# Kernel optimization log

Measured on AMD Instinct MI355X. Metric: run time of the kernel, lower is better.

The kernel has to match this reference:

```python
import jax, jax.numpy as jnp
import numpy as np

B, L, PD, DIM, H, DH, DEPTH, MLP, NIMG, NCLS, TH = 2, 2048, 768, 512, 8, 64, 2, 2048, 4, 1000, 32


def _ln(x, g):
    # bias-free LayerNorm (beta buffer is zeros), eps matches torch F.layer_norm
    mu = jnp.mean(x, axis=-1, keepdims=True)
    var = jnp.var(x, axis=-1, keepdims=True)
    return (x - mu) / jnp.sqrt(var + 1e-5) * g


def _rms(x, g):
    # F.normalize(dim=-1) * sqrt(dim_head) * gamma; x: [b,h,n,dh], g: [h,1,dh]
    n = jnp.linalg.norm(x, axis=-1, keepdims=True)
    return x / jnp.maximum(n, 1e-12) * (DH ** 0.5) * g


def _attn(x, context, mask, ln_g, qg, kg, Wq, Wkv, Wo):
    b, n = x.shape[0], x.shape[1]
    xn = _ln(x, ln_g)
    kv = xn if context is None else context  # context is NOT pre-normed (matches source)
    m = kv.shape[1]
    q = (xn @ Wq).reshape(b, n, H, DH).transpose(0, 2, 1, 3)   # [b,h,n,dh]
    k, v = jnp.split(kv @ Wkv, 2, axis=-1)
    k = k.reshape(b, m, H, DH).transpose(0, 2, 1, 3)
    v = v.reshape(b, m, H, DH).transpose(0, 2, 1, 3)
    q = _rms(q, qg)
    k = _rms(k, kg)
    dots = jnp.einsum('bhid,bhjd->bhij', q, k)  # no 1/sqrt(d): QK-RMSNorm carries the scale
    neg = -jnp.finfo(dots.dtype).max
    dots = jnp.where(mask, dots, neg)
    a = jax.nn.softmax(dots, axis=-1)
    out = jnp.einsum('bhij,bhjd->bhid', a, v)
    out = out.transpose(0, 2, 1, 3).reshape(b, n, H * DH)
    return out @ Wo


def _forward(patches, ln_pe1_g, W_pe, b_pe, ln_pe2_g, pos_h_emb, pos_w_emb,
             attn_ln_g, q_g, k_g, Wq, Wkv, Wo, ff_ln_g, W1, b1, W2, b2,
             final_ln_g, pool_q, pool_ln_g, pool_q_g, pool_k_g,
             pool_Wq, pool_Wkv, pool_Wo, head_ln_g, W_head,
             pos_h, pos_w, image_ids):
    # patch embedding: LN -> Linear -> LN, then factorized 2D pos embed
    x = _ln(patches, ln_pe1_g) @ W_pe + b_pe
    x = _ln(x, ln_pe2_g)
    x = x + pos_h_emb[pos_h] + pos_w_emb[pos_w]
    # block-diagonal attention mask: tokens attend only within their image
    mask = (image_ids[:, None, :, None] == image_ids[:, None, None, :])  # [B,1,L,L]
    for i in range(DEPTH):
        x = _attn(x, None, mask, attn_ln_g[i], q_g[i], k_g[i], Wq[i], Wkv[i], Wo[i]) + x
        h = _ln(x, ff_ln_g[i]) @ W1[i] + b1[i]
        h = jax.nn.gelu(h, approximate=False)
        x = h @ W2[i] + b2[i] + x
    x = _ln(x, final_ln_g)
    # attention pooling: one learned query per packed image
    queries = jnp.broadcast_to(pool_q, (B, NIMG, DIM))
    pmask = (jnp.arange(NIMG)[None, None, :, None] == image_ids[:, None, None, :])  # [B,1,NIMG,L]
    pooled = _attn(queries, x, pmask, pool_ln_g, pool_q_g, pool_k_g, pool_Wq, pool_Wkv, pool_Wo) + queries
    return _ln(pooled, head_ln_g) @ W_head  # [B, NIMG, NCLS]


def setup_inputs() -> dict:
    key = jax.random.key(0)
    ks = jax.random.split(key, 16)
    s = 0.02
    inp = {}
    inp['patches'] = jax.random.normal(ks[0], (B, L, PD), jnp.float32)
    inp['pos_h'] = jax.random.randint(ks[1], (B, L), 0, TH)
    inp['pos_w'] = jax.random.randint(ks[2], (B, L), 0, TH)
    inp['image_ids'] = jnp.sort(jax.random.randint(ks[3], (B, L), 0, NIMG), axis=-1)
    inp['ln_pe1_g'] = jnp.ones((PD,), jnp.float32)
    inp['W_pe'] = jax.random.normal(ks[4], (PD, DIM), jnp.float32) * s
    inp['b_pe'] = jnp.zeros((DIM,), jnp.float32)
    inp['ln_pe2_g'] = jnp.ones((DIM,), jnp.float32)
    inp['pos_h_emb'] = jax.random.normal(ks[5], (TH, DIM), jnp.float32)
    inp['pos_w_emb'] = jax.random.normal(ks[6], (TH, DIM), jnp.float32)
    inp['attn_ln_g'] = jnp.ones((DEPTH, DIM), jnp.float32)
    inp['q_g'] = jnp.ones((DEPTH, H, 1, DH), jnp.float32)
    inp['k_g'] = jnp.ones((DEPTH, H, 1, DH), jnp.float32)
    inp['Wq'] = jax.random.normal(ks[7], (DEPTH, DIM, H * DH), jnp.float32) * s
    inp['Wkv'] = jax.random.normal(ks[8], (DEPTH, DIM, 2 * H * DH), jnp.float32) * s
    inp['Wo'] = jax.random.normal(ks[9], (DEPTH, H * DH, DIM), jnp.float32) * s
    inp['ff_ln_g'] = jnp.ones((DEPTH, DIM), jnp.float32)
    inp['W1'] = jax.random.normal(ks[10], (DEPTH, DIM, MLP), jnp.float32) * s
    inp['b1'] = jnp.zeros((DEPTH, MLP), jnp.float32)
    inp['W2'] = jax.random.normal(ks[11], (DEPTH, MLP, DIM), jnp.float32) * s
    inp['b2'] = jnp.zeros((DEPTH, DIM), jnp.float32)
    inp['final_ln_g'] = jnp.ones((DIM,), jnp.float32)
    inp['pool_q'] = jax.random.normal(ks[12], (DIM,), jnp.float32)
    inp['pool_ln_g'] = jnp.ones((DIM,), jnp.float32)
    inp['pool_q_g'] = jnp.ones((H, 1, DH), jnp.float32)
    inp['pool_k_g'] = jnp.ones((H, 1, DH), jnp.float32)
    inp['pool_Wq'] = jax.random.normal(ks[13], (DIM, H * DH), jnp.float32) * s
    inp['pool_Wkv'] = jax.random.normal(ks[14], (DIM, 2 * H * DH), jnp.float32) * s
    inp['pool_Wo'] = jax.random.normal(ks[15], (H * DH, DIM), jnp.float32) * s
    inp['head_ln_g'] = jnp.ones((DIM,), jnp.float32)
    inp['W_head'] = jax.random.normal(jax.random.fold_in(key, 99), (DIM, NCLS), jnp.float32) * s
    return inp


def reference(patches, pos_h, pos_w, image_ids, ln_pe1_g, W_pe, b_pe, ln_pe2_g,
              pos_h_emb, pos_w_emb, attn_ln_g, q_g, k_g, Wq, Wkv, Wo, ff_ln_g,
              W1, b1, W2, b2, final_ln_g, pool_q, pool_ln_g, pool_q_g, pool_k_g,
              pool_Wq, pool_Wkv, pool_Wo, head_ln_g, W_head):
    return _forward(patches, ln_pe1_g, W_pe, b_pe, ln_pe2_g, pos_h_emb, pos_w_emb,
                    attn_ln_g, q_g, k_g, Wq, Wkv, Wo, ff_ln_g, W1, b1, W2, b2,
                    final_ln_g, pool_q, pool_ln_g, pool_q_g, pool_k_g,
                    pool_Wq, pool_Wkv, pool_Wo, head_ln_g, W_head,
                    pos_h, pos_w, image_ids)
```

## Files before the change

kernel.cpp:

```cpp
#include <hip/hip_runtime.h>
#include <hip/hip_bf16.h>
#include <cfloat>
#include <math.h>

#define BB 2
#define LL 2048
#define PD 768
#define DIM 512
#define HH 8
#define DH 64
#define DEPTH 2
#define MLP 2048
#define NIMG 4
#define NCLS 1000
#define ROWS (BB*LL)
#define NEGBIG (-1e30f)

typedef __hip_bfloat16 bf16;
typedef __bf16 v8bf __attribute__((ext_vector_type(8)));
typedef float f32x4 __attribute__((ext_vector_type(4)));

__device__ __forceinline__ float ldin(const void* p, size_t i, int bf) {
    return bf ? __bfloat162float(((const bf16*)p)[i]) : ((const float*)p)[i];
}
__device__ __forceinline__ float lda(const float* p, size_t i) { return p[i]; }
__device__ __forceinline__ float lda(const bf16* p, size_t i) { return __bfloat162float(p[i]); }
__device__ __forceinline__ void st(float* p, size_t i, float v) { p[i] = v; }
__device__ __forceinline__ void st(bf16* p, size_t i, float v) { p[i] = __float2bfloat16(v); }
__device__ __forceinline__ unsigned short f2bf(float x) {
    return __builtin_bit_cast(unsigned short, __float2bfloat16(x));
}
__device__ __forceinline__ float us2f(unsigned short u) {
    return __bfloat162float(__builtin_bit_cast(bf16, u));
}

__device__ __forceinline__ void stage16(const void* gsrc, void* ldst)
{
    __builtin_amdgcn_global_load_lds(
        (const __attribute__((address_space(1))) unsigned int*)(unsigned long long)gsrc,
        (__attribute__((address_space(3))) unsigned int*)(unsigned int)(unsigned long long)ldst,
        16, 0, 0);
}

__global__ void detect_dtype_kernel(const void* ones, int* flag)
{
    if (threadIdx.x == 0 && blockIdx.x == 0)
        *flag = (((const unsigned*)ones)[0] == 0x3F803F80u) ? 1 : 0;
}

__global__ void wconv_kernel(const void* __restrict__ W, int K, int N,
                             bf16* __restrict__ out, const int* dtf)
{
    __shared__ float t[32][33];
    const int bf = *dtf;
    const size_t zoff = (size_t)blockIdx.z * K * N;
    const int kb = blockIdx.y * 32, nb = blockIdx.x * 32;
    const int tx = threadIdx.x, ty = threadIdx.y;
    #pragma unroll
    for (int u = 0; u < 4; ++u)
        t[ty + 8 * u][tx] = ldin(W, zoff + (size_t)(kb + ty + 8 * u) * N + nb + tx, bf);
    __syncthreads();
    #pragma unroll
    for (int u = 0; u < 4; ++u)
        out[zoff + (size_t)(nb + ty + 8 * u) * K + kb + tx] = __float2bfloat16(t[tx][ty + 8 * u]);
}

template<int RAWIN, typename TOUT>
__global__ void ln_kernel(const void* __restrict__ in, const void* __restrict__ g, size_t goff,
                          TOUT* __restrict__ out, int D, const int* dtf)
{
    __shared__ float red[16];
    const int bf = *dtf;
    const int row = blockIdx.x, tid = threadIdx.x;
    const size_t base = (size_t)row * D;
    float s = 0.f, ss = 0.f;
    for (int d = tid; d < D; d += blockDim.x) {
        float v = RAWIN ? ldin(in, base + d, bf) : ((const float*)in)[base + d];
        s += v; ss += v * v;
    }
    for (int o = 32; o; o >>= 1) { s += __shfl_xor(s, o); ss += __shfl_xor(ss, o); }
    const int wid = tid >> 6, lane = tid & 63, nw = blockDim.x >> 6;
    if (lane == 0) { red[wid] = s; red[8 + wid] = ss; }
    __syncthreads();
    if (tid == 0) {
        float a = 0.f, b = 0.f;
        for (int w = 0; w < nw; ++w) { a += red[w]; b += red[8 + w]; }
        red[0] = a; red[8] = b;
    }
    __syncthreads();
    const float mean = red[0] / D;
    const float var  = red[8] / D - mean * mean;
    const float rstd = rsqrtf(var + 1e-5f);
    for (int d = tid; d < D; d += blockDim.x) {
        float v = RAWIN ? ldin(in, base + d, bf) : ((const float*)in)[base + d];
        st(out, base + d, (v - mean) * rstd * ldin(g, goff + d, bf));
    }
}

__global__ void ln_pos_kernel(float* __restrict__ x, const void* __restrict__ g,
                              const void* __restrict__ phe, const void* __restrict__ pwe,
                              const int* __restrict__ ph, const int* __restrict__ pw,
                              const int* dtf)
{
    __shared__ float red[16];
    const int bf = *dtf;
    const int row = blockIdx.x, tid = threadIdx.x;
    const size_t base = (size_t)row * DIM;
    float s = 0.f, ss = 0.f;
    for (int d = tid; d < DIM; d += 256) { float v = x[base + d]; s += v; ss += v * v; }
    for (int o = 32; o; o >>= 1) { s += __shfl_xor(s, o); ss += __shfl_xor(ss, o); }
    const int wid = tid >> 6, lane = tid & 63;
    if (lane == 0) { red[wid] = s; red[8 + wid] = ss; }
    __syncthreads();
    if (tid == 0) {
        float a = 0.f, b = 0.f;
        for (int w = 0; w < 4; ++w) { a += red[w]; b += red[8 + w]; }
        red[0] = a; red[8] = b;
    }
    __syncthreads();
    const float mean = red[0] / DIM;
    const float var  = red[8] / DIM - mean * mean;
    const float rstd = rsqrtf(var + 1e-5f);
    const size_t hoff = (size_t)ph[row] * DIM, woff = (size_t)pw[row] * DIM;
    for (int d = tid; d < DIM; d += 256) {
        float v = (x[base + d] - mean) * rstd * ldin(g, d, bf)
                + ldin(phe, hoff + d, bf) + ldin(pwe, woff + d, bf);
        x[base + d] = v;
    }
}

#define GM 128
#define GN 64
#define GK 64

template<typename TO, int EPI>
__global__ void mgemm_kernel(const bf16* __restrict__ A, const bf16* __restrict__ Wt,
                             const void* __restrict__ bias, size_t boff,
                             const float* __restrict__ resid, TO* __restrict__ out,
                             int M, int N, int K, int kc, int gelu, const int* dtf)
{
    __shared__ __align__(16) unsigned short As[GM][GK];
    __shared__ __align__(16) unsigned short Bs[GN][GK];
    const int tid = threadIdx.x;
    const int w = tid >> 6, l = tid & 63, g = l >> 4, c = l & 15;
    const int wm = (w >> 1) * 64, wn = (w & 1) * 32;
    const int m0 = blockIdx.y * GM, n0 = blockIdx.x * GN;
    const int kbeg = blockIdx.z * kc, kend = kbeg + kc;
    const int lrow = l >> 3, lcol = (l & 7) * 8;

    f32x4 acc[4][2] = {};

    for (int k0 = kbeg; k0 < kend; k0 += GK) {
        __syncthreads();
        #pragma unroll
        for (int u = 0; u < 4; ++u) {
            const int rr = 32 * w + 8 * u;
            stage16(A + (size_t)(m0 + rr + lrow) * K + k0 + lcol, &As[rr][0]);
        }
        #pragma unroll
        for (int u = 0; u < 2; ++u) {
            const int rr = 16 * w + 8 * u;
            stage16(Wt + (size_t)(n0 + rr + lrow) * K + k0 + lcol, &Bs[rr][0]);
        }
        __syncthreads();
        #pragma unroll
        for (int kk = 0; kk < GK; kk += 32) {
            v8bf av[4], bv[2];
            #pragma unroll
            for (int i = 0; i < 4; ++i) av[i] = *(const v8bf*)&As[wm + i * 16 + c][kk + 8 * g];
            #pragma unroll
            for (int j = 0; j < 2; ++j) bv[j] = *(const v8bf*)&Bs[wn + j * 16 + c][kk + 8 * g];
            #pragma unroll
            for (int i = 0; i < 4; ++i)
                #pragma unroll
                for (int j = 0; j < 2; ++j)
                    acc[i][j] = __builtin_amdgcn_mfma_f32_16x16x32_bf16(av[i], bv[j], acc[i][j], 0, 0, 0);
        }
    }

    if (EPI == 0) {
        float* po = (float*)out + (size_t)blockIdx.z * M * N;
        #pragma unroll
        for (int i = 0; i < 4; ++i) {
            const int rb = m0 + wm + i * 16 + 4 * g;
            #pragma unroll
            for (int j = 0; j < 2; ++j) {
                const int col = n0 + wn + j * 16 + c;
                #pragma unroll
                for (int r = 0; r < 4; ++r)
                    po[(size_t)(rb + r) * N + col] = acc[i][j][r];
            }
        }
    } else {
        const int bf = *dtf;
        #pragma unroll
        for (int i = 0; i < 4; ++i) {
            const int rb = m0 + wm + i * 16 + 4 * g;
            #pragma unroll
            for (int j = 0; j < 2; ++j) {
                const int col = n0 + wn + j * 16 + c;
                const float bvl = bias ? ldin(bias, boff + col, bf) : 0.f;
                #pragma unroll
                for (int r = 0; r < 4; ++r) {
                    float v = acc[i][j][r] + bvl;
                    if (gelu) v = 0.5f * v * (1.f + erff(v * 0.70710678118654752f));
                    if (resid) v += resid[(size_t)(rb + r) * N + col];
                    st(out, (size_t)(rb + r) * N + col, v);
                }
            }
        }
    }
}

template<typename TO>
__global__ void mcomb_kernel(const float* __restrict__ part, int S, const void* __restrict__ bias,
                             size_t boff, const float* __restrict__ resid, TO* __restrict__ out,
                             size_t MN, int N, int gelu, const int* dtf)
{
    const size_t idx = (size_t)blockIdx.x * 256 + threadIdx.x;
    if (idx >= MN) return;
    float v = 0.f;
    for (int s = 0; s < S; ++s) v += part[(size_t)s * MN + idx];
    const int bf = *dtf;
    if (bias) v += ldin(bias, boff + (int)(idx % N), bf);
    if (gelu) v = 0.5f * v * (1.f + erff(v * 0.70710678118654752f));
    if (resid) v += resid[idx];
    st(out, idx, v);
}

__global__ void comb_ln_kernel(const float* __restrict__ part, int S,
                               const void* __restrict__ bias, size_t boff,
                               float* __restrict__ x, const void* __restrict__ g, size_t goff,
                               bf16* __restrict__ xb, const int* dtf)
{
    __shared__ float red[16];
    const int bf = *dtf;
    const int row = blockIdx.x, tid = threadIdx.x;
    const size_t base = (size_t)row * DIM;
    float v[2];
    float s = 0.f, ss = 0.f;
    #pragma unroll
    for (int u = 0; u < 2; ++u) {
        const int d = tid + 256 * u;
        float a = 0.f;
        for (int sc = 0; sc < S; ++sc) a += part[(size_t)sc * ROWS * DIM + base + d];
        if (bias) a += ldin(bias, boff + d, bf);
        a += x[base + d];
        x[base + d] = a;
        v[u] = a; s += a; ss += a * a;
    }
    for (int o = 32; o; o >>= 1) { s += __shfl_xor(s, o); ss += __shfl_xor(ss, o); }
    const int wid = tid >> 6, lane = tid & 63;
    if (lane == 0) { red[wid] = s; red[8 + wid] = ss; }
    __syncthreads();
    if (tid == 0) {
        float a = 0.f, b = 0.f;
        for (int w2 = 0; w2 < 4; ++w2) { a += red[w2]; b += red[8 + w2]; }
        red[0] = a; red[8] = b;
    }
    __syncthreads();
    const float mean = red[0] / DIM;
    const float var  = red[8] / DIM - mean * mean;
    const float rstd = rsqrtf(var + 1e-5f);
    #pragma unroll
    for (int u = 0; u < 2; ++u) {
        const int d = tid + 256 * u;
        xb[base + d] = __float2bfloat16((v[u] - mean) * rstd * ldin(g, goff + d, bf));
    }
}

#define TS 16
template<typename TA, typename TO>
__global__ void gemm_kernel(const TA* __restrict__ A, const void* __restrict__ W, size_t woff,
                            const void* __restrict__ bias, size_t boff,
                            const float* __restrict__ resid, TO* __restrict__ out,
                            int M, int N, int K, int gelu, const int* dtf)
{
    __shared__ float As[TS][TS + 1];
    __shared__ float Bs[TS][TS + 1];
    const int bf = *dtf;
    const int tx = threadIdx.x, ty = threadIdx.y;
    const int col = blockIdx.x * TS + tx;
    const int row = blockIdx.y * TS + ty;
    float acc = 0.f;
    for (int k0 = 0; k0 < K; k0 += TS) {
        const int ka = k0 + tx;
        As[ty][tx] = (row < M && ka < K) ? lda(A, (size_t)row * K + ka) : 0.f;
        const int kb = k0 + ty;
        Bs[ty][tx] = (col < N && kb < K) ? ldin(W, woff + (size_t)kb * N + col, bf) : 0.f;
        __syncthreads();
        #pragma unroll
        for (int kk = 0; kk < TS; ++kk) acc = fmaf(As[ty][kk], Bs[kk][tx], acc);
        __syncthreads();
    }
    if (row < M && col < N) {
        if (bias) acc += ldin(bias, boff + col, bf);
        if (gelu) acc = 0.5f * acc * (1.f + erff(acc * 0.70710678118654752f));
        if (resid) acc += resid[(size_t)row * N + col];
        st(out, (size_t)row * N + col, acc);
    }
}

__global__ void rms_kernel(float* __restrict__ buf, const void* __restrict__ g, size_t goff,
                           int stride, int colbase, const int* dtf)
{
    const int bf = *dtf;
    const int r = blockIdx.x, h = blockIdx.y, lane = threadIdx.x;
    float* p = buf + (size_t)r * stride + colbase + h * DH;
    const float v = p[lane];
    float ss = v * v;
    for (int o = 32; o; o >>= 1) ss += __shfl_xor(ss, o);
    const float norm = sqrtf(ss);
    const float sc = 8.0f / fmaxf(norm, 1e-12f);
    p[lane] = v * sc * ldin(g, goff + h * DH + lane, bf);
}

__global__ void rms2_kernel(bf16* __restrict__ buf, int stride,
                            const void* __restrict__ g0, size_t g0off,
                            int base1, const void* __restrict__ g1, size_t g1off,
                            int nslot, const int* dtf)
{
    const int bf = *dtf;
    const int tid = threadIdx.x;
    const int s = tid >> 4, li = tid & 15;
    if (s >= nslot) return;
    const int h = s & 7;
    const int colbase = (s < 8) ? 0 : base1;
    const void* g = (s < 8) ? g0 : g1;
    const size_t go = ((s < 8) ? g0off : g1off) + h * DH + li * 4;
    bf16* p = buf + (size_t)blockIdx.x * stride + colbase + h * DH + li * 4;
    ushort4 v = *(const ushort4*)p;
    const float f0 = us2f(v.x), f1 = us2f(v.y), f2 = us2f(v.z), f3 = us2f(v.w);
    float ss = f0 * f0 + f1 * f1 + f2 * f2 + f3 * f3;
    ss += __shfl_xor(ss, 8); ss += __shfl_xor(ss, 4);
    ss += __shfl_xor(ss, 2); ss += __shfl_xor(ss, 1);
    const float sc = 8.0f / fmaxf(sqrtf(ss), 1e-12f);
    ushort4 o;
    o.x = f2bf(f0 * sc * ldin(g, go + 0, bf));
    o.y = f2bf(f1 * sc * ldin(g, go + 1, bf));
    o.z = f2bf(f2 * sc * ldin(g, go + 2, bf));
    o.w = f2bf(f3 * sc * ldin(g, go + 3, bf));
    *(ushort4*)p = o;
}

#define QT 64
#define KT 64
#define LP 72

__global__ void flash_attn_kernel(const bf16* __restrict__ q, int qstr,
                                  const bf16* __restrict__ kpt, const bf16* __restrict__ vpt,
                                  int kvstr, const int* __restrict__ ids,
                                  bf16* __restrict__ out)
{
    __shared__ __align__(16) unsigned short Qs[QT][LP];
    __shared__ __align__(16) unsigned short Ks[KT][LP];
    __shared__ __align__(16) unsigned short Vt[DH][LP];
    __shared__ __align__(16) unsigned short Ps[QT][LP];
    __shared__ __align__(16) int ids_s[KT];
    __shared__ __align__(16) int qids_s[QT];
    __shared__ int range_s[2];

    const int tid = threadIdx.x;
    const int h = blockIdx.y, b = blockIdx.z;
    const int qb = blockIdx.x * QT;
    const int w = tid >> 6, l = tid & 63, g = l >> 4, c = l & 15;

    {
        const int r = tid >> 2, c0 = (tid & 3) << 4;
        const bf16* qp = q + (size_t)(b * LL + qb + r) * qstr + h * DH + c0;
        *(int4*)&Qs[r][c0]     = *(const int4*)qp;
        *(int4*)&Qs[r][c0 + 8] = *(const int4*)(qp + 8);
        if (tid < QT) qids_s[tid] = ids[b * LL + qb + tid];
    }
    if (tid == 0) {
        const int* bp = ids + b * LL;
        const int qlo = bp[qb], qhi = bp[qb + QT - 1];
        int lo = 0, hi = LL;
        while (lo < hi) { int mid = (lo + hi) >> 1; if (bp[mid] < qlo) lo = mid + 1; else hi = mid; }
        range_s[0] = lo;
        int lo2 = 0, hi2 = LL;
        while (lo2 < hi2) { int mid = (lo2 + hi2) >> 1; if (bp[mid] <= qhi) lo2 = mid + 1; else hi2 = mid; }
        range_s[1] = lo2;
    }
    __syncthreads();

    const int myid = qids_s[16 * w + c];
    const v8bf qf0 = *(const v8bf*)&Qs[16 * w + c][8 * g];
    const v8bf qf1 = *(const v8bf*)&Qs[16 * w + c][8 * g + 32];
    const int kb_start = (range_s[0] / KT) * KT;
    const int kb_end = range_s[1];

    f32x4 o[4];
    #pragma unroll
    for (int dt = 0; dt < 4; ++dt) o[dt] = (f32x4){0.f, 0.f, 0.f, 0.f};
    float mr = NEGBIG, lr = 0.f;

    for (int kb = kb_start; kb < kb_end; kb += KT) {
        __syncthreads();
        {
            const int r = tid >> 2, c0 = (tid & 3) << 4;
            const bf16* kp = kpt + (size_t)(b * LL + kb + r) * kvstr + h * DH + c0;
            *(int4*)&Ks[r][c0]     = *(const int4*)kp;
            *(int4*)&Ks[r][c0 + 8] = *(const int4*)(kp + 8);
        }
        {
            const int kp2 = (tid & 31) * 2, db = (tid >> 5) * 8;
            const bf16* v0p = vpt + (size_t)(b * LL + kb + kp2) * kvstr + h * DH + db;
            const bf16* v1p = v0p + kvstr;
            const ushort4 a0 = *(const ushort4*)v0p;
            const ushort4 a1 = *(const ushort4*)(v0p + 4);
            const ushort4 b0 = *(const ushort4*)v1p;
            const ushort4 b1 = *(const ushort4*)(v1p + 4);
            const unsigned short* ap0 = (const unsigned short*)&a0;
            const unsigned short* ap1 = (const unsigned short*)&a1;
            const unsigned short* bp0 = (const unsigned short*)&b0;
            const unsigned short* bp1 = (const unsigned short*)&b1;
            #pragma unroll
            for (int j = 0; j < 4; ++j) {
                *(unsigned int*)&Vt[db + j][kp2]     = (unsigned)ap0[j] | ((unsigned)bp0[j] << 16);
                *(unsigned int*)&Vt[db + 4 + j][kp2] = (unsigned)ap1[j] | ((unsigned)bp1[j] << 16);
            }
        }
        if (tid < KT) ids_s[tid] = ids[b * LL + kb + tid];
        __syncthreads();

        f32x4 stt[4];
        #pragma unroll
        for (int t = 0; t < 4; ++t) {
            stt[t] = (f32x4){0.f, 0.f, 0.f, 0.f};
            v8bf kf0 = *(const v8bf*)&Ks[16 * t + c][8 * g];
            v8bf kf1 = *(const v8bf*)&Ks[16 * t + c][8 * g + 32];
            stt[t] = __builtin_amdgcn_mfma_f32_16x16x32_bf16(kf0, qf0, stt[t], 0, 0, 0);
            stt[t] = __builtin_amdgcn_mfma_f32_16x16x32_bf16(kf1, qf1, stt[t], 0, 0, 0);
        }

        float sv[16]; int mk[16];
        float tmax = NEGBIG;
        #pragma unroll
        for (int t = 0; t < 4; ++t) {
            int4 iv = *(const int4*)&ids_s[16 * t + 4 * g];
            const int* ivp = (const int*)&iv;
            #pragma unroll
            for (int r = 0; r < 4; ++r) {
                float s = stt[t][r];
                int m = (ivp[r] == myid);
                sv[4 * t + r] = s; mk[4 * t + r] = m;
                if (m) tmax = fmaxf(tmax, s);
            }
        }
        tmax = fmaxf(tmax, __shfl_xor(tmax, 16));
        tmax = fmaxf(tmax, __shfl_xor(tmax, 32));
        const float mnew = fmaxf(mr, tmax);
        const float al = __expf(mr - mnew);
        float tsum = 0.f;
        #pragma unroll
        for (int t = 0; t < 4; ++t) {
            ushort4 pk;
            unsigned short* pp = (unsigned short*)&pk;
            #pragma unroll
            for (int r = 0; r < 4; ++r) {
                float p = mk[4 * t + r] ? __expf(sv[4 * t + r] - mnew) : 0.f;
                tsum += p;
                pp[r] = f2bf(p);
            }
            *(ushort4*)&Ps[16 * w + c][16 * t + 4 * g] = pk;
        }
        tsum += __shfl_xor(tsum, 16);
        tsum += __shfl_xor(tsum, 32);
        lr = lr * al + tsum;
        mr = mnew;

        const float a0 = __shfl(al, 4 * g + 0);
        const float a1 = __shfl(al, 4 * g + 1);
        const float a2 = __shfl(al, 4 * g + 2);
        const float a3 = __shfl(al, 4 * g + 3);
        #pragma unroll
        for (int dt = 0; dt < 4; ++dt) {
            o[dt][0] *= a0; o[dt][1] *= a1; o[dt][2] *= a2; o[dt][3] *= a3;
        }

        const v8bf pf0 = *(const v8bf*)&Ps[16 * w + c][8 * g];
        const v8bf pf1 = *(const v8bf*)&Ps[16 * w + c][8 * g + 32];
        #pragma unroll
        for (int dt = 0; dt < 4; ++dt) {
            v8bf vf0 = *(const v8bf*)&Vt[16 * dt + c][8 * g];
            v8bf vf1 = *(const v8bf*)&Vt[16 * dt + c][8 * g + 32];
            o[dt] = __builtin_amdgcn_mfma_f32_16x16x32_bf16(pf0, vf0, o[dt], 0, 0, 0);
            o[dt] = __builtin_amdgcn_mfma_f32_16x16x32_bf16(pf1, vf1, o[dt], 0, 0, 0);
        }
    }

    const float li0 = 1.f / __shfl(lr, 4 * g + 0);
    const float li1 = 1.f / __shfl(lr, 4 * g + 1);
    const float li2 = 1.f / __shfl(lr, 4 * g + 2);
    const float li3 = 1.f / __shfl(lr, 4 * g + 3);
    #pragma unroll
    for (int dt = 0; dt < 4; ++dt) {
        bf16* op = out + (size_t)(b * LL + qb + 16 * w) * DIM + h * DH + 16 * dt + c;
        op[(size_t)(4 * g + 0) * DIM] = __float2bfloat16(o[dt][0] * li0);
        op[(size_t)(4 * g + 1) * DIM] = __float2bfloat16(o[dt][1] * li1);
        op[(size_t)(4 * g + 2) * DIM] = __float2bfloat16(o[dt][2] * li2);
        op[(size_t)(4 * g + 3) * DIM] = __float2bfloat16(o[dt][3] * li3);
    }
}

#define PCH 16
#define PCK (LL / PCH)

__global__ void pool_attn_part_kernel(const float* __restrict__ q, const bf16* __restrict__ kv,
                                      int kvs, const int* __restrict__ ids,
                                      float* __restrict__ ppm, float* __restrict__ ppl,
                                      float* __restrict__ ppo)
{
    const int iq = blockIdx.x & (NIMG - 1), ch = blockIdx.x >> 2;
    const int h = blockIdx.y, b = blockIdx.z;
    const int tid = threadIdx.x;
    const int qrow = b * NIMG + iq;
    const int j0 = ch * PCK;
    __shared__ float qs[DH];
    __shared__ float s[PCK];

    qs[tid] = q[(size_t)qrow * DIM + h * DH + tid];
    __syncthreads();
    #pragma unroll
    for (int u = 0; u < 2; ++u) {
        const int j = j0 + tid + 64 * u;
        const bf16* kp = kv + (size_t)(b * LL + j) * kvs + h * DH;
        float d = 0.f;
        #pragma unroll
        for (int t = 0; t < DH; t += 8) {
            int4 kvv = *(const int4*)&kp[t];
            const unsigned short* uu = (const unsigned short*)&kvv;
            #pragma unroll
            for (int z = 0; z < 8; ++z) d = fmaf(qs[t + z], us2f(uu[z]), d);
        }
        s[tid + 64 * u] = (ids[b * LL + j] == iq) ? d : NEGBIG;
    }
    __syncthreads();
    float m = fmaxf(s[tid], s[tid + 64]);
    for (int o = 32; o; o >>= 1) m = fmaxf(m, __shfl_xor(m, o));
    const float p0 = __expf(s[tid] - m), p1 = __expf(s[tid + 64] - m);
    float ls = p0 + p1;
    for (int o = 32; o; o >>= 1) ls += __shfl_xor(ls, o);
    s[tid] = p0; s[tid + 64] = p1;
    __syncthreads();
    float acc = 0.f;
    for (int jj = 0; jj < PCK; ++jj)
        acc += s[jj] * __bfloat162float(kv[(size_t)(b * LL + j0 + jj) * kvs + DIM + h * DH + tid]);
    const int p = ((b * HH + h) * NIMG + iq) * PCH + ch;
    if (tid == 0) { ppm[p] = m; ppl[p] = ls; }
    ppo[(size_t)p * DH + tid] = acc;
}

__global__ void pool_attn_comb_kernel(const float* __restrict__ ppm, const float* __restrict__ ppl,
                                      const float* __restrict__ ppo, float* __restrict__ out)
{
    const int iq = blockIdx.x, h = blockIdx.y, b = blockIdx.z;
    const int d = threadIdx.x;
    const int pb = ((b * HH + h) * NIMG + iq) * PCH;
    float mstar = NEGBIG;
    #pragma unroll
    for (int ch = 0; ch < PCH; ++ch) mstar = fmaxf(mstar, ppm[pb + ch]);
    float lsum = 0.f, osum = 0.f;
    #pragma unroll
    for (int ch = 0; ch < PCH; ++ch) {
        const float w = __expf(ppm[pb + ch] - mstar);
        lsum += ppl[pb + ch] * w;
        osum += ppo[(size_t)(pb + ch) * DH + d] * w;
    }
    out[(size_t)(b * NIMG + iq) * DIM + h * DH + d] = osum / lsum;
}

__global__ void fill_q_kernel(float* __restrict__ queries, const void* __restrict__ pool_q,
                              const int* dtf)
{
    const int bf = *dtf;
    const int idx = blockIdx.x * blockDim.x + threadIdx.x;
    if (idx < BB * NIMG * DIM) queries[idx] = ldin(pool_q, idx % DIM, bf);
}

__global__ void write_out_kernel(const float* __restrict__ in, void* __restrict__ out, int n,
                                 const int* dtf)
{
    const int bf = *dtf;
    const int idx = blockIdx.x * blockDim.x + threadIdx.x;
    if (idx < n) {
        if (bf) ((bf16*)out)[idx] = __float2bfloat16(in[idx]);
        else    ((float*)out)[idx] = in[idx];
    }
}

extern "C" void kernel_launch(void* const* d_in, const int* in_sizes, int n_in,
                              void* d_out, int out_size, void* d_ws, size_t ws_size,
                              hipStream_t stream)
{
    const void* patches   = d_in[0];
    const int*  pos_h     = (const int*) d_in[1];
    const int*  pos_w     = (const int*) d_in[2];
    const int*  image_ids = (const int*) d_in[3];
    const void* ln_pe1_g  = d_in[4];
    const void* W_pe      = d_in[5];
    const void* b_pe      = d_in[6];
    const void* ln_pe2_g  = d_in[7];
    const void* pos_h_emb = d_in[8];
    const void* pos_w_emb = d_in[9];
    const void* attn_ln_g = d_in[10];
    const void* q_g       = d_in[11];
    const void* k_g       = d_in[12];
    const void* Wq        = d_in[13];
    const void* Wkv       = d_in[14];
    const void* Wo        = d_in[15];
    const void* ff_ln_g   = d_in[16];
    const void* W1        = d_in[17];
    const void* b1        = d_in[18];
    const void* W2        = d_in[19];
    const void* b2        = d_in[20];
    const void* final_ln_g= d_in[21];
    const void* pool_q    = d_in[22];
    const void* pool_ln_g = d_in[23];
    const void* pool_q_g  = d_in[24];
    const void* pool_k_g  = d_in[25];
    const void* pool_Wq   = d_in[26];
    const void* pool_Wkv  = d_in[27];
    const void* pool_Wo   = d_in[28];
    const void* head_ln_g = d_in[29];
    const void* W_head    = d_in[30];

    char* p = (char*)d_ws;
    int* flag = (int*)p;                         p += 256;
    float* x   = (float*)p;                      p += (size_t)ROWS * DIM * 4;
    bf16* xb   = (bf16*)p;                       p += (size_t)ROWS * PD * 2;
    bf16* qkvb = (bf16*)p;  bf16* hb = qkvb;     p += (size_t)ROWS * MLP * 2;
    bf16* wpeT  = (bf16*)p;                      p += (size_t)DIM * PD * 2;
    bf16* wqT   = (bf16*)p;                      p += (size_t)DEPTH * DIM * DIM * 2;
    bf16* wkvT  = (bf16*)p;                      p += (size_t)DEPTH * 2 * DIM * DIM * 2;
    bf16* woT   = (bf16*)p;                      p += (size_t)DEPTH * DIM * DIM * 2;
    bf16* w1T   = (bf16*)p;                      p += (size_t)DEPTH * MLP * DIM * 2;
    bf16* w2T   = (bf16*)p;                      p += (size_t)DEPTH * DIM * MLP * 2;
    bf16* pkvT  = (bf16*)p;                      p += (size_t)2 * DIM * DIM * 2;
    float* queries = (float*)p;                  p += 4096 * 4;
    float* qp      = (float*)p;                  p += 4096 * 4;
    float* pattn   = (float*)p;                  p += 4096 * 4;
    float* pooled  = (float*)p;                  p += 4096 * 4;
    bf16*  pln     = (bf16*)p;                   p += 4096 * 2;
    float* hout    = (float*)p;                  p += 8192 * 4;
    float* ppm     = (float*)p;                  p += 1024 * 4;
    float* ppl     = (float*)p;                  p += 1024 * 4;
    float* ppo     = (float*)p;                  p += (size_t)1024 * DH * 4;
    float* part    = (float*)p;                  p += (size_t)4 * ROWS * DIM * 4;

    const dim3 blk256(256);
    const dim3 blkG(TS, TS);
    const dim3 blkT(32, 8);

    detect_dtype_kernel<<<1, 1, 0, stream>>>(ln_pe1_g, flag);

    wconv_kernel<<<dim3(DIM / 32, PD / 32, 1), blkT, 0, stream>>>(W_pe, PD, DIM, wpeT, flag);
    wconv_kernel<<<dim3(DIM / 32, DIM / 32, DEPTH), blkT, 0, stream>>>(Wq, DIM, DIM, wqT, flag);
    wconv_kernel<<<dim3(2 * DIM / 32, DIM / 32, DEPTH), blkT, 0, stream>>>(Wkv, DIM, 2 * DIM, wkvT, flag);
    wconv_kernel<<<dim3(DIM / 32, DIM / 32, DEPTH), blkT, 0, stream>>>(Wo, DIM, DIM, woT, flag);
    wconv_kernel<<<dim3(MLP / 32, DIM / 32, DEPTH), blkT, 0, stream>>>(W1, DIM, MLP, w1T, flag);
    wconv_kernel<<<dim3(DIM / 32, MLP / 32, DEPTH), blkT, 0, stream>>>(W2, MLP, DIM, w2T, flag);
    wconv_kernel<<<dim3(2 * DIM / 32, DIM / 32, 1), blkT, 0, stream>>>(pool_Wkv, DIM, 2 * DIM, pkvT, flag);

    ln_kernel<1, bf16><<<ROWS, blk256, 0, stream>>>(patches, ln_pe1_g, 0, xb, PD, flag);
    mgemm_kernel<float, 0><<<dim3(DIM / GN, ROWS / GM, 2), blk256, 0, stream>>>(
        xb, wpeT, nullptr, 0, nullptr, part, ROWS, DIM, PD, PD / 2, 0, flag);
    mcomb_kernel<float><<<(ROWS * DIM + 255) / 256, blk256, 0, stream>>>(
        part, 2, b_pe, 0, nullptr, x, (size_t)ROWS * DIM, DIM, 0, flag);
    ln_pos_kernel<<<ROWS, blk256, 0, stream>>>(x, ln_pe2_g, pos_h_emb, pos_w_emb, pos_h, pos_w, flag);
    ln_kernel<0, bf16><<<ROWS, blk256, 0, stream>>>(x, attn_ln_g, 0, xb, DIM, flag);

    for (int i = 0; i < DEPTH; ++i) {
        mgemm_kernel<bf16, 1><<<dim3(DIM / GN, ROWS / GM, 1), blk256, 0, stream>>>(
            xb, wqT + (size_t)i * DIM * DIM, nullptr, 0, nullptr, qkvb,
            ROWS, DIM, DIM, DIM, 0, flag);
        mgemm_kernel<bf16, 1><<<dim3(2 * DIM / GN, ROWS / GM, 1), blk256, 0, stream>>>(
            xb, wkvT + (size_t)i * 2 * DIM * DIM, nullptr, 0, nullptr, qkvb + (size_t)ROWS * DIM,
            ROWS, 2 * DIM, DIM, DIM, 0, flag);
        rms2_kernel<<<ROWS, blk256, 0, stream>>>(
            qkvb, DIM, q_g, (size_t)i * HH * DH, 0, nullptr, 0, 8, flag);
        rms2_kernel<<<ROWS, blk256, 0, stream>>>(
            qkvb + (size_t)ROWS * DIM, 2 * DIM, k_g, (size_t)i * HH * DH, 0, nullptr, 0, 8, flag);
        flash_attn_kernel<<<dim3(LL / QT, HH, BB), blk256, 0, stream>>>(
            qkvb, DIM, qkvb + (size_t)ROWS * DIM, qkvb + (size_t)ROWS * DIM + DIM, 2 * DIM,
            image_ids, xb);
        mgemm_kernel<float, 0><<<dim3(DIM / GN, ROWS / GM, 2), blk256, 0, stream>>>(
            xb, woT + (size_t)i * DIM * DIM, nullptr, 0, nullptr, part,
            ROWS, DIM, DIM, DIM / 2, 0, flag);
        comb_ln_kernel<<<ROWS, blk256, 0, stream>>>(
            part, 2, nullptr, 0, x, ff_ln_g, (size_t)i * DIM, xb, flag);
        mgemm_kernel<bf16, 1><<<dim3(MLP / GN, ROWS / GM, 1), blk256, 0, stream>>>(
            xb, w1T + (size_t)i * MLP * DIM, b1, (size_t)i * MLP, nullptr, hb,
            ROWS, MLP, DIM, DIM, 1, flag);
        mgemm_kernel<float, 0><<<dim3(DIM / GN, ROWS / GM, 4), blk256, 0, stream>>>(
            hb, w2T + (size_t)i * DIM * MLP, nullptr, 0, nullptr, part,
            ROWS, DIM, MLP, MLP / 4, 0, flag);
        const void* gnext = (i + 1 < DEPTH) ? attn_ln_g : final_ln_g;
        const size_t gnoff = (i + 1 < DEPTH) ? (size_t)(i + 1) * DIM : 0;
        comb_ln_kernel<<<ROWS, blk256, 0, stream>>>(
            part, 4, b2, (size_t)i * DIM, x, gnext, gnoff, xb, flag);
    }

    fill_q_kernel<<<(BB * NIMG * DIM + 255) / 256, blk256, 0, stream>>>(queries, pool_q, flag);
    ln_kernel<0, bf16><<<BB * NIMG, blk256, 0, stream>>>(queries, pool_ln_g, 0, pln, DIM, flag);
    gemm_kernel<bf16, float><<<dim3(DIM / TS, 1), blkG, 0, stream>>>(
        pln, pool_Wq, 0, nullptr, 0, nullptr, qp, BB * NIMG, DIM, DIM, 0, flag);
    mgemm_kernel<bf16, 1><<<dim3(2 * DIM / GN, ROWS / GM, 1), blk256, 0, stream>>>(
        xb, pkvT, nullptr, 0, nullptr, qkvb, ROWS, 2 * DIM, DIM, DIM, 0, flag);
    rms_kernel<<<dim3(BB * NIMG, HH), dim3(64), 0, stream>>>(
        qp, pool_q_g, 0, DIM, 0, flag);
    rms2_kernel<<<ROWS, blk256, 0, stream>>>(
        qkvb, 2 * DIM, pool_k_g, 0, 0, nullptr, 0, 8, flag);
    pool_attn_part_kernel<<<dim3(NIMG * PCH, HH, BB), dim3(64), 0, stream>>>(
        qp, qkvb, 2 * DIM, image_ids, ppm, ppl, ppo);
    pool_attn_comb_kernel<<<dim3(NIMG, HH, BB), dim3(64), 0, stream>>>(ppm, ppl, ppo, pattn);
    gemm_kernel<float, float><<<dim3(DIM / TS, 1), blkG, 0, stream>>>(
        pattn, pool_Wo, 0, nullptr, 0, queries, pooled, BB * NIMG, DIM, DIM, 0, flag);

    ln_kernel<0, bf16><<<BB * NIMG, blk256, 0, stream>>>(pooled, head_ln_g, 0, pln, DIM, flag);
    gemm_kernel<bf16, float><<<dim3((NCLS + TS - 1) / TS, 1), blkG, 0, stream>>>(
        pln, W_head, 0, nullptr, 0, nullptr, hout, BB * NIMG, NCLS, DIM, 0, flag);
    write_out_kernel<<<(BB * NIMG * NCLS + 255) / 256, blk256, 0, stream>>>(
        hout, d_out, BB * NIMG * NCLS, flag);
}
```

Measured before the change: 505.4 us.

## Fuse Q and KV projections into one QKV GEMM and remap attention blocks

Concatenates transposed Wq and Wkv into a single interleaved QKV weight so one GEMM writes a row-major [rows, 3*DIM] buffer, and a single rms2 launch normalizes both q and k heads. The flash attention kernel switches to a 1D grid with a swizzled block-to-(batch, head, q-tile) mapping, which spreads consecutive blocks across heads and q tiles. This is meant to cut launch count, give larger GEMM tiles grids, and balance the per-tile workload of the block-diagonal mask across compute units. It relies on rms2_kernel's second-tensor path being correct with the new stride and offsets.

```diff
diff --git a/kernel.cpp b/kernel.cpp
--- a/kernel.cpp
+++ b/kernel.cpp
@@ -14,6 +14,7 @@
 #define NIMG 4
 #define NCLS 1000
 #define ROWS (BB*LL)
+#define QKV (3*DIM)
 #define NEGBIG (-1e30f)
 
 typedef __hip_bfloat16 bf16;
@@ -48,21 +49,23 @@
         *flag = (((const unsigned*)ones)[0] == 0x3F803F80u) ? 1 : 0;
 }
 
-__global__ void wconv_kernel(const void* __restrict__ W, int K, int N,
-                             bf16* __restrict__ out, const int* dtf)
+__global__ void wconv_kernel(const void* __restrict__ W, int K, int N, size_t inStride,
+                             bf16* __restrict__ out, size_t outOff, size_t outStride,
+                             const int* dtf)
 {
     __shared__ float t[32][33];
     const int bf = *dtf;
-    const size_t zoff = (size_t)blockIdx.z * K * N;
+    const size_t zin = (size_t)blockIdx.z * inStride;
+    const size_t zout = outOff + (size_t)blockIdx.z * outStride;
     const int kb = blockIdx.y * 32, nb = blockIdx.x * 32;
     const int tx = threadIdx.x, ty = threadIdx.y;
     #pragma unroll
     for (int u = 0; u < 4; ++u)
-        t[ty + 8 * u][tx] = ldin(W, zoff + (size_t)(kb + ty + 8 * u) * N + nb + tx, bf);
+        t[ty + 8 * u][tx] = ldin(W, zin + (size_t)(kb + ty + 8 * u) * N + nb + tx, bf);
     __syncthreads();
     #pragma unroll
     for (int u = 0; u < 4; ++u)
-        out[zoff + (size_t)(nb + ty + 8 * u) * K + kb + tx] = __float2bfloat16(t[tx][ty + 8 * u]);
+        out[zout + (size_t)(nb + ty + 8 * u) * K + kb + tx] = __float2bfloat16(t[tx][ty + 8 * u]);
 }
 
 template<int RAWIN, typename TOUT>
@@ -361,8 +364,11 @@
     __shared__ int range_s[2];
 
     const int tid = threadIdx.x;
-    const int h = blockIdx.y, b = blockIdx.z;
-    const int qb = blockIdx.x * QT;
+    const int bid = blockIdx.x;
+    const int s0 = (bid & 7) * 64 + (bid >> 3);
+    const int qb = (s0 & 31) * QT;
+    const int h = (s0 >> 5) & 7;
+    const int b = s0 >> 8;
     const int w = tid >> 6, l = tid & 63, g = l >> 4, c = l & 15;
 
     {
@@ -632,8 +638,7 @@
     bf16* xb   = (bf16*)p;                       p += (size_t)ROWS * PD * 2;
     bf16* qkvb = (bf16*)p;  bf16* hb = qkvb;     p += (size_t)ROWS * MLP * 2;
     bf16* wpeT  = (bf16*)p;                      p += (size_t)DIM * PD * 2;
-    bf16* wqT   = (bf16*)p;                      p += (size_t)DEPTH * DIM * DIM * 2;
-    bf16* wkvT  = (bf16*)p;                      p += (size_t)DEPTH * 2 * DIM * DIM * 2;
+    bf16* wqkvT = (bf16*)p;                      p += (size_t)DEPTH * QKV * DIM * 2;
     bf16* woT   = (bf16*)p;                      p += (size_t)DEPTH * DIM * DIM * 2;
     bf16* w1T   = (bf16*)p;                      p += (size_t)DEPTH * MLP * DIM * 2;
     bf16* w2T   = (bf16*)p;                      p += (size_t)DEPTH * DIM * MLP * 2;
@@ -655,13 +660,20 @@
 
     detect_dtype_kernel<<<1, 1, 0, stream>>>(ln_pe1_g, flag);
 
-    wconv_kernel<<<dim3(DIM / 32, PD / 32, 1), blkT, 0, stream>>>(W_pe, PD, DIM, wpeT, flag);
-    wconv_kernel<<<dim3(DIM / 32, DIM / 32, DEPTH), blkT, 0, stream>>>(Wq, DIM, DIM, wqT, flag);
-    wconv_kernel<<<dim3(2 * DIM / 32, DIM / 32, DEPTH), blkT, 0, stream>>>(Wkv, DIM, 2 * DIM, wkvT, flag);
-    wconv_kernel<<<dim3(DIM / 32, DIM / 32, DEPTH), blkT, 0, stream>>>(Wo, DIM, DIM, woT, flag);
-    wconv_kernel<<<dim3(MLP / 32, DIM / 32, DEPTH), blkT, 0, stream>>>(W1, DIM, MLP, w1T, flag);
-    wconv_kernel<<<dim3(DIM / 32, MLP / 32, DEPTH), blkT, 0, stream>>>(W2, MLP, DIM, w2T, flag);
-    wconv_kernel<<<dim3(2 * DIM / 32, DIM / 32, 1), blkT, 0, stream>>>(pool_Wkv, DIM, 2 * DIM, pkvT, flag);
+    wconv_kernel<<<dim3(DIM / 32, PD / 32, 1), blkT, 0, stream>>>(
+        W_pe, PD, DIM, 0, wpeT, 0, 0, flag);
+    wconv_kernel<<<dim3(DIM / 32, DIM / 32, DEPTH), blkT, 0, stream>>>(
+        Wq, DIM, DIM, (size_t)DIM * DIM, wqkvT, 0, (size_t)QKV * DIM, flag);
+    wconv_kernel<<<dim3(2 * DIM / 32, DIM / 32, DEPTH), blkT, 0, stream>>>(
+        Wkv, DIM, 2 * DIM, (size_t)DIM * 2 * DIM, wqkvT, (size_t)DIM * DIM, (size_t)QKV * DIM, flag);
+    wconv_kernel<<<dim3(DIM / 32, DIM / 32, DEPTH), blkT, 0, stream>>>(
+        Wo, DIM, DIM, (size_t)DIM * DIM, woT, 0, (size_t)DIM * DIM, flag);
+    wconv_kernel<<<dim3(MLP / 32, DIM / 32, DEPTH), blkT, 0, stream>>>(
+        W1, DIM, MLP, (size_t)DIM * MLP, w1T, 0, (size_t)MLP * DIM, flag);
+    wconv_kernel<<<dim3(DIM / 32, MLP / 32, DEPTH), blkT, 0, stream>>>(
+        W2, MLP, DIM, (size_t)MLP * DIM, w2T, 0, (size_t)DIM * MLP, flag);
+    wconv_kernel<<<dim3(2 * DIM / 32, DIM / 32, 1), blkT, 0, stream>>>(
+        pool_Wkv, DIM, 2 * DIM, 0, pkvT, 0, 0, flag);
 
     ln_kernel<1, bf16><<<ROWS, blk256, 0, stream>>>(patches, ln_pe1_g, 0, xb, PD, flag);
     mgemm_kernel<float, 0><<<dim3(DIM / GN, ROWS / GM, 2), blk256, 0, stream>>>(
@@ -672,19 +684,13 @@
     ln_kernel<0, bf16><<<ROWS, blk256, 0, stream>>>(x, attn_ln_g, 0, xb, DIM, flag);
 
     for (int i = 0; i < DEPTH; ++i) {
-        mgemm_kernel<bf16, 1><<<dim3(DIM / GN, ROWS / GM, 1), blk256, 0, stream>>>(
-            xb, wqT + (size_t)i * DIM * DIM, nullptr, 0, nullptr, qkvb,
-            ROWS, DIM, DIM, DIM, 0, flag);
-        mgemm_kernel<bf16, 1><<<dim3(2 * DIM / GN, ROWS / GM, 1), blk256, 0, stream>>>(
-            xb, wkvT + (size_t)i * 2 * DIM * DIM, nullptr, 0, nullptr, qkvb + (size_t)ROWS * DIM,
-            ROWS, 2 * DIM, DIM, DIM, 0, flag);
+        mgemm_kernel<bf16, 1><<<dim3(QKV / GN, ROWS / GM, 1), blk256, 0, stream>>>(
+            xb, wqkvT + (size_t)i * QKV * DIM, nullptr, 0, nullptr, qkvb,
+            ROWS, QKV, DIM, DIM, 0, flag);
         rms2_kernel<<<ROWS, blk256, 0, stream>>>(
-            qkvb, DIM, q_g, (size_t)i * HH * DH, 0, nullptr, 0, 8, flag);
-        rms2_kernel<<<ROWS, blk256, 0, stream>>>(
-            qkvb + (size_t)ROWS * DIM, 2 * DIM, k_g, (size_t)i * HH * DH, 0, nullptr, 0, 8, flag);
-        flash_attn_kernel<<<dim3(LL / QT, HH, BB), blk256, 0, stream>>>(
-            qkvb, DIM, qkvb + (size_t)ROWS * DIM, qkvb + (size_t)ROWS * DIM + DIM, 2 * DIM,
-            image_ids, xb);
+            qkvb, QKV, q_g, (size_t)i * HH * DH, DIM, k_g, (size_t)i * HH * DH, 16, flag);
+        flash_attn_kernel<<<dim3(512), blk256, 0, stream>>>(
+            qkvb, QKV, qkvb + DIM, qkvb + 2 * DIM, QKV, image_ids, xb);
         mgemm_kernel<float, 0><<<dim3(DIM / GN, ROWS / GM, 2), blk256, 0, stream>>>(
             xb, woT + (size_t)i * DIM * DIM, nullptr, 0, nullptr, part,
             ROWS, DIM, DIM, DIM / 2, 0, flag);
```

Result: faster. 473.4 us (-6.3%).
